# Optimization experiments

Measured on AMD Instinct MI355X. Metric: run time of the kernel, lower is better.

The kernel has to match this reference:

```python
import jax, jax.numpy as jnp
import numpy as np

Q_N, S_N, U_N = 5000, 1000, 2000          # questions, skills, users
NQ = NS = NU = NQ2 = 8                     # neighbor fan-outs
D = 100                                    # emb_dim
AGG_HOPS = 3
RANK_K = 10
S_PER_Q = 4                                # skills per question in qs_table
B, T = 32, 100
NEG = -1e30


def linear(x, W, b):
    return x @ W + b


def _forward(fl, it):
    (uq_table, emb_q, emb_q2, emb_s, emb_u, emb_r,
     w1_q, w2_q, w_c, w_p, w_n,
     lstm_Wih, lstm_Whh, lstm_bih, lstm_bhh,
     fusion_W, fusion_b, agg_W, agg_b, agg_last_W, agg_last_b,
     query_W, query_b, key_W, key_b, attn_W, attn_b) = fl
    (user, question, response, mask,
     q_neighbors, s_neighbors, u_neighbors, q_neighbors_2, skill_idx_table) = it

    K_all = emb_q[question]  # [B,T,D] question embeddings for recap scoring

    def build_nodes(root, tabA, tabB):
        # multi-hop neighbor id gather: [B], [B,n0], [B,n0,n1], [B,n0,n1,n2]
        nodes = [root]
        for i in range(AGG_HOPS):
            tab = tabA if i % 2 == 0 else tabB
            nodes.append(tab[nodes[-1]])
        return nodes

    def aggregate(nodes, embA, embB, weighted):
        embs = [(embA if i % 2 == 0 else embB)[n] for i, n in enumerate(nodes)]
        for i in range(AGG_HOPS):
            for j in range(AGG_HOPS - i):
                nb = embs[j + 1]
                if weighted:  # uq branch: edge weights from dense uq_table
                    self_ids, nb_ids = nodes[j], nodes[j + 1]
                    exp_self = jnp.broadcast_to(self_ids[..., None], nb_ids.shape)
                    uid = exp_self if j % 2 == 0 else nb_ids
                    qid = nb_ids if j % 2 == 0 else exp_self
                    w = uq_table[uid, qid]  # [..., 3]
                    fw = w_c * w[..., 0:1] + w_p * w[..., 1:2] + w_n * w[..., 2:3]
                    nb = nb * fw
                s = nb.mean(axis=-2) + embs[j]
                embs[j] = jax.nn.relu(linear(s, agg_W[j], agg_b[j]))
        return jax.nn.relu(linear(embs[0], agg_last_W, agg_last_b))

    def predict(qs_concat, hist, hist_valid):
        # GIKT-style bi-attention readout (source truncated; see notes)
        k = linear(qs_concat, key_W, key_b)    # [B,Nq,D]
        q = linear(hist, query_W, query_b)     # [B,Nh,D]
        Nq, Nh = k.shape[1], q.shape[1]
        feat = jnp.concatenate([
            jnp.broadcast_to(k[:, :, None, :], (B, Nq, Nh, D)),
            jnp.broadcast_to(q[:, None, :, :], (B, Nq, Nh, D))], axis=-1)
        logits = (feat @ attn_W + attn_b)[..., 0]          # [B,Nq,Nh]
        logits = jnp.where(hist_valid[:, None, :], logits, NEG)
        alpha = jax.nn.softmax(logits.reshape(B, -1), axis=1).reshape(B, Nq, Nh)
        inner = jnp.einsum('bqd,bhd->bqh', qs_concat, hist)
        return jax.nn.sigmoid(jnp.sum(alpha * inner, axis=(1, 2)))

    def step(carry, t):
        h, c, state_hist = carry
        m = mask[:, t][:, None]
        u_t, q_t, r_t = user[:, t], question[:, t], response[:, t]
        emb_qt = jnp.where(m, aggregate(build_nodes(q_t, q_neighbors, s_neighbors), emb_q, emb_s, False), emb_q[q_t])
        emb_qt2 = jnp.where(m, aggregate(build_nodes(u_t, u_neighbors, q_neighbors_2), emb_u, emb_q2, True), emb_q2[q_t])
        emb_hat = w1_q * emb_qt + w2_q * emb_qt2
        e_t = jax.nn.relu(linear(jnp.concatenate([emb_hat, emb_r[r_t]], axis=1), fusion_W, fusion_b))
        # LSTMCell (torch gate order i,f,g,o); dropout is identity in eval
        gates = e_t @ lstm_Wih + lstm_bih + h @ lstm_Whh + lstm_bhh
        ig, fg, gg, og = jnp.split(gates, 4, axis=1)
        c_n = jax.nn.sigmoid(fg) * c + jax.nn.sigmoid(ig) * jnp.tanh(gg)
        h_n = jax.nn.sigmoid(og) * jnp.tanh(c_n)
        h = jnp.where(m, h_n, h)
        c = jnp.where(m, c_n, c)
        state_hist = jax.lax.dynamic_update_slice_in_dim(state_hist, h[:, None, :], t, axis=1)
        # recap: question + related skills, current state + top-k history
        q_next = question[:, t + 1]
        emb_qnext = emb_q[q_next]
        qs_concat = jnp.concatenate([emb_qnext[:, None, :], emb_s[skill_idx_table[q_next]]], axis=1)  # [B,1+S_PER_Q,D]
        scores = jnp.einsum('btd,bd->bt', K_all, emb_qnext)
        scores = jnp.where(jnp.arange(T)[None, :] < t, scores, NEG)  # only past steps
        top_s, idx = jax.lax.top_k(scores, RANK_K)
        sel = jnp.take_along_axis(state_hist, idx[:, :, None], axis=1)  # [B,K,D]
        hist = jnp.concatenate([h[:, None, :], sel], axis=1)             # [B,K+1,D]
        hist_valid = jnp.concatenate([jnp.ones((B, 1), bool), top_s > NEG / 2], axis=1)
        return (h, c, state_hist), predict(qs_concat, hist, hist_valid)

    init = (jnp.zeros((B, D), jnp.float32), jnp.zeros((B, D), jnp.float32),
            jnp.zeros((B, T, D), jnp.float32))
    _, ys = jax.lax.scan(jax.checkpoint(step), init, jnp.arange(T - 1))
    return jnp.zeros((B, T), jnp.float32).at[:, 1:].set(ys.T)


def _p(k, shape, scale=0.1):
    return scale * jax.random.normal(k, shape, dtype=jnp.float32)


def setup_inputs():
    key = jax.random.key(0)
    ks = jax.random.split(key, 24)
    rng = np.random.default_rng(0)
    # qs_table with exactly S_PER_Q distinct skills per question -> static skill index table
    qs_idx = np.argsort(rng.random((Q_N, S_N)), axis=1)[:, :S_PER_Q]
    return dict(
        user=jax.random.randint(ks[0], (B, T), 0, U_N),
        question=jax.random.randint(ks[1], (B, T), 0, Q_N),
        response=jax.random.randint(ks[2], (B, T), 0, 2),
        mask=jnp.ones((B, T), dtype=bool),
        q_neighbors=jax.random.randint(ks[3], (Q_N, NQ), 0, S_N),
        s_neighbors=jax.random.randint(ks[4], (S_N, NS), 0, Q_N),
        u_neighbors=jax.random.randint(ks[5], (U_N, NU), 0, Q_N),
        q_neighbors_2=jax.random.randint(ks[6], (Q_N, NQ2), 0, U_N),
        skill_idx_table=jnp.asarray(qs_idx, dtype=jnp.int32),
        uq_table=jax.random.uniform(ks[7], (U_N, Q_N, 3), dtype=jnp.float32),
        emb_q=_p(ks[8], (Q_N, D)), emb_q2=_p(ks[9], (Q_N, D)),
        emb_s=_p(ks[10], (S_N, D)), emb_u=_p(ks[11], (U_N, D)), emb_r=_p(ks[12], (2, D)),
        w1_q=jnp.asarray(0.5, jnp.float32), w2_q=jnp.asarray(0.5, jnp.float32),
        w_c=jnp.asarray(0.33, jnp.float32), w_p=jnp.asarray(0.33, jnp.float32), w_n=jnp.asarray(0.33, jnp.float32),
        lstm_Wih=_p(ks[13], (D, 4 * D)), lstm_Whh=_p(ks[14], (D, 4 * D)),
        lstm_bih=jnp.zeros(4 * D, jnp.float32), lstm_bhh=jnp.zeros(4 * D, jnp.float32),
        fusion_W=_p(ks[15], (2 * D, D)), fusion_b=jnp.zeros(D, jnp.float32),
        agg_W=_p(ks[16], (AGG_HOPS, D, D)), agg_b=jnp.zeros((AGG_HOPS, D), jnp.float32),
        agg_last_W=_p(ks[17], (D, D)), agg_last_b=jnp.zeros(D, jnp.float32),
        query_W=_p(ks[18], (D, D)), query_b=jnp.zeros(D, jnp.float32),
        key_W=_p(ks[19], (D, D)), key_b=jnp.zeros(D, jnp.float32),
        attn_W=_p(ks[20], (2 * D, 1)), attn_b=jnp.zeros(1, jnp.float32),
    )


def reference(user, question, response, mask, q_neighbors, s_neighbors, u_neighbors,
              q_neighbors_2, skill_idx_table, uq_table, emb_q, emb_q2, emb_s, emb_u, emb_r,
              w1_q, w2_q, w_c, w_p, w_n, lstm_Wih, lstm_Whh, lstm_bih, lstm_bhh,
              fusion_W, fusion_b, agg_W, agg_b, agg_last_W, agg_last_b,
              query_W, query_b, key_W, key_b, attn_W, attn_b):
    fl = (uq_table, emb_q, emb_q2, emb_s, emb_u, emb_r,
          w1_q, w2_q, w_c, w_p, w_n,
          lstm_Wih, lstm_Whh, lstm_bih, lstm_bhh,
          fusion_W, fusion_b, agg_W, agg_b, agg_last_W, agg_last_b,
          query_W, query_b, key_W, key_b, attn_W, attn_b)
    it = (user, question, response, mask,
          q_neighbors, s_neighbors, u_neighbors, q_neighbors_2, skill_idx_table)
    return _forward(fl, it)
```

## Files before the change

### kernel.cpp

```cpp
#include <hip/hip_runtime.h>
#include <math.h>

#define Q_N 5000
#define S_N 1000
#define U_N 2000
#define D   100
#define B   32
#define T   100
#define NBT (B*(T-1))
#define NEG_F (-1e30f)

#define NB_Z2Q ((Q_N+15)/16)
#define NB_Z2U ((U_N+15)/16)
#define NB_Y1Q ((S_N+15)/16)
#define NB_Y1U ((Q_N+15)/16)
#define WB16_U16 (13*400*8)
#define WB16_F   (WB16_U16/2)
#define NB_MK ((NBT+255)/256)
#define NB_PK ((WB16_U16+255)/256)

#define GPROJ_SZ (NBT*4*D)
#define H_SZ     (B*T*D)
#define QAGG_SZ  (Q_N*D)
#define UAGG_SZ  (U_N*D)
#define Z2Q_SZ   (Q_N*D)
#define Z2U_SZ   (U_N*D)
#define Y1Q_SZ   (S_N*D)
#define Y1U_SZ   (Q_N*D)

__device__ __forceinline__ void fma4(float4& a, float s, const float4 w) {
    a.x = fmaf(s, w.x, a.x); a.y = fmaf(s, w.y, a.y);
    a.z = fmaf(s, w.z, a.z); a.w = fmaf(s, w.w, a.w);
}
__device__ __forceinline__ float4 relu4(float4 v) {
    v.x = v.x > 0.f ? v.x : 0.f; v.y = v.y > 0.f ? v.y : 0.f;
    v.z = v.z > 0.f ? v.z : 0.f; v.w = v.w > 0.f ? v.w : 0.f;
    return v;
}
__device__ __forceinline__ float4 add4(float4 a, float4 b) {
    a.x += b.x; a.y += b.y; a.z += b.z; a.w += b.w; return a;
}
__device__ __forceinline__ float b2f_lo(unsigned u) { return __uint_as_float(u << 16); }
__device__ __forceinline__ float b2f_hi(unsigned u) { return __uint_as_float(u & 0xffff0000u); }

template<int K>
__device__ __forceinline__ void mv100_b256(const float* __restrict__ W,
                                           const float* __restrict__ bias,
                                           const float* __restrict__ src,
                                           float* __restrict__ dst,
                                           float* __restrict__ part)
{
    const int tid = threadIdx.x;
    const int c4  = tid & 31;
    const int ks  = tid >> 5;
    const int col0 = (4*c4 < 96) ? 4*c4 : 96;
    float4 acc = {0.f,0.f,0.f,0.f};
#pragma unroll 2
    for (int d = ks*4; d < K; d += 32) {
        const float4 sv = *(const float4*)&src[d];
        const float4 w0 = *(const float4*)&W[(d+0)*D + col0];
        const float4 w1 = *(const float4*)&W[(d+1)*D + col0];
        const float4 w2 = *(const float4*)&W[(d+2)*D + col0];
        const float4 w3 = *(const float4*)&W[(d+3)*D + col0];
        fma4(acc, sv.x, w0); fma4(acc, sv.y, w1);
        fma4(acc, sv.z, w2); fma4(acc, sv.w, w3);
    }
    *(float4*)&part[ks*D + col0] = acc;
    __syncthreads();
    if (tid < D) {
        float v = bias[tid];
#pragma unroll
        for (int k = 0; k < 8; ++k) v += part[k*D + tid];
        dst[tid] = v > 0.f ? v : 0.f;
    }
    __syncthreads();
}

struct __align__(16) Stage16 {
    float x[16*D];
    int   nb[128];
    float fw[128];
};

template<int UQ_MODE>
__device__ __forceinline__ void stage16(Stage16& sh, int row0, int N,
        const float* __restrict__ selfEmb, const float* __restrict__ nbEmb,
        const int* __restrict__ tab,
        const float* __restrict__ uq, float wc, float wp, float wn,
        const float* __restrict__ W, const float* __restrict__ bias,
        float* __restrict__ out)
{
    const int tid = threadIdx.x;
    if (tid < 128) {
        const int i = tid >> 3, k = tid & 7;
        int v = row0 + i; if (v >= N) v = N - 1;
        const int nbv = tab[v*8 + k];
        sh.nb[tid] = nbv;
        float f = 0.125f;
        if (UQ_MODE == 1) {
            const float* w = &uq[(v*Q_N + nbv)*3];
            f = 0.125f*(wc*w[0] + wp*w[1] + wn*w[2]);
        } else if (UQ_MODE == 2) {
            const float* w = &uq[(nbv*Q_N + v)*3];
            f = 0.125f*(wc*w[0] + wp*w[1] + wn*w[2]);
        }
        sh.fw[tid] = f;
    }
    __syncthreads();
    const int c4   = tid & 31;
    const int rowg = tid >> 5;
    const int col0 = (4*c4 < 96) ? 4*c4 : 96;
#pragma unroll
    for (int rr = 0; rr < 2; ++rr) {
        const int i = rowg + 8*rr;
        int v = row0 + i; if (v >= N) v = N - 1;
        float4 acc = *(const float4*)&selfEmb[v*D + col0];
#pragma unroll
        for (int k = 0; k < 8; ++k)
            fma4(acc, sh.fw[i*8 + k], *(const float4*)&nbEmb[sh.nb[i*8 + k]*D + col0]);
        *(float4*)&sh.x[i*D + col0] = acc;
    }
    __syncthreads();
    float4 a0 = {0.f,0.f,0.f,0.f}, a1 = {0.f,0.f,0.f,0.f};
#pragma unroll 1
    for (int d = 0; d < D; d += 4) {
        const float4 w0 = *(const float4*)&W[(d+0)*D + col0];
        const float4 w1 = *(const float4*)&W[(d+1)*D + col0];
        const float4 w2 = *(const float4*)&W[(d+2)*D + col0];
        const float4 w3 = *(const float4*)&W[(d+3)*D + col0];
        const float4 s0 = *(const float4*)&sh.x[rowg*D + d];
        const float4 s1 = *(const float4*)&sh.x[(rowg+8)*D + d];
        fma4(a0, s0.x, w0); fma4(a0, s0.y, w1); fma4(a0, s0.z, w2); fma4(a0, s0.w, w3);
        fma4(a1, s1.x, w0); fma4(a1, s1.y, w1); fma4(a1, s1.z, w2); fma4(a1, s1.w, w3);
    }
    const float4 bb = *(const float4*)&bias[col0];
    {
        int v = row0 + rowg; if (v >= N) v = N - 1;
        *(float4*)&out[v*D + col0] = relu4(add4(a0, bb));
        v = row0 + rowg + 8; if (v >= N) v = N - 1;
        *(float4*)&out[v*D + col0] = relu4(add4(a1, bb));
    }
}

__global__ __launch_bounds__(256, 6)
void kStageA(const int* __restrict__ qnb, const int* __restrict__ snb,
             const int* __restrict__ unb, const int* __restrict__ qnb2,
             const float* __restrict__ emb_q, const float* __restrict__ emb_q2,
             const float* __restrict__ emb_s, const float* __restrict__ emb_u,
             const float* __restrict__ uq,
             const float* __restrict__ wcp, const float* __restrict__ wpp,
             const float* __restrict__ wnp,
             const float* __restrict__ aggW, const float* __restrict__ aggB,
             float* __restrict__ z2q, float* __restrict__ z2u,
             float* __restrict__ y1q0, float* __restrict__ y1u0)
{
    __shared__ Stage16 sh;
    const float wc = wcp[0], wp = wpp[0], wn = wnp[0];
    int b = blockIdx.x;
    if (b < NB_Z2Q) {
        stage16<0>(sh, b*16, Q_N, emb_q, emb_s, qnb, uq, wc, wp, wn,
                   aggW + 2*D*D, aggB + 2*D, z2q);
        return;
    }
    b -= NB_Z2Q;
    if (b < NB_Z2U) {
        stage16<1>(sh, b*16, U_N, emb_u, emb_q2, unb, uq, wc, wp, wn,
                   aggW + 2*D*D, aggB + 2*D, z2u);
        return;
    }
    b -= NB_Z2U;
    if (b < NB_Y1Q) {
        stage16<0>(sh, b*16, S_N, emb_s, emb_q, snb, uq, wc, wp, wn,
                   aggW + 1*D*D, aggB + 1*D, y1q0);
        return;
    }
    b -= NB_Y1Q;
    stage16<2>(sh, b*16, Q_N, emb_q2, emb_u, qnb2, uq, wc, wp, wn,
               aggW + 1*D*D, aggB + 1*D, y1u0);
}

__global__ __launch_bounds__(256, 6)
void kStageB(const int* __restrict__ snb, const int* __restrict__ qnb2,
             const float* __restrict__ uq,
             const float* __restrict__ wcp, const float* __restrict__ wpp,
             const float* __restrict__ wnp,
             const float* __restrict__ aggW, const float* __restrict__ aggB,
             const float* __restrict__ z2q, const float* __restrict__ z2u,
             const float* __restrict__ y1q0, const float* __restrict__ y1u0,
             float* __restrict__ y1q1, float* __restrict__ y1u1)
{
    __shared__ Stage16 sh;
    const float wc = wcp[0], wp = wpp[0], wn = wnp[0];
    int b = blockIdx.x;
    if (b < NB_Y1Q) {
        stage16<0>(sh, b*16, S_N, y1q0, z2q, snb, uq, wc, wp, wn,
                   aggW + 1*D*D, aggB + 1*D, y1q1);
        return;
    }
    b -= NB_Y1Q;
    stage16<2>(sh, b*16, Q_N, y1u0, z2u, qnb2, uq, wc, wp, wn,
               aggW + 1*D*D, aggB + 1*D, y1u1);
}

__global__ void kMarkInit(int* __restrict__ marks)
{
    const int i = blockIdx.x*256 + threadIdx.x;
    if (i < Q_N + U_N) marks[i] = 0;
}

__global__ __launch_bounds__(256)
void kSetup(const int* __restrict__ question, const int* __restrict__ user,
            int* __restrict__ qmark, int* __restrict__ umark,
            const float* __restrict__ Whh, ushort* __restrict__ wb,
            const float* __restrict__ keyW, const float* __restrict__ queryW,
            const float* __restrict__ attnW,
            float* __restrict__ vk, float* __restrict__ vq)
{
    int bkt = blockIdx.x;
    const int tid = threadIdx.x;
    if (bkt < NB_MK) {
        const int bt = bkt*256 + tid;
        if (bt < NBT) {
            const int b = bt / (T-1), t = bt % (T-1);
            qmark[question[b*T + t]] = 1;
            umark[user[b*T + t]] = 1;
        }
        return;
    }
    bkt -= NB_MK;
    if (bkt < NB_PK) {
        const int i = bkt*256 + tid;
        if (i < WB16_U16) {
            const int j  = i & 7;
            const int mc = i >> 3;
            const int m  = mc / 400;
            const int col = mc - m*400;
            const int d  = 8*m + j;
            ushort v = 0;
            if (d < D) {
                unsigned u = __float_as_uint(Whh[d*4*D + col]);
                const unsigned lsb = (u >> 16) & 1u;
                u += 0x7fffu + lsb;
                v = (ushort)(u >> 16);
            }
            wb[i] = v;
        }
        return;
    }
    if (tid < D) {
        float a = 0.f;
        for (int e = 0; e < D; ++e) a = fmaf(keyW[tid*D + e], attnW[e], a);
        vk[tid] = a;
    } else if (tid < 2*D) {
        const int d = tid - D;
        float a = 0.f;
        for (int e = 0; e < D; ++e) a = fmaf(queryW[d*D + e], attnW[D + e], a);
        vq[d] = a;
    }
}

struct __align__(16) RootSh {
    float e0[D];
    float part[8*D];
    int   nb[8];
    float fw[8];
};

template<bool WEIGHTED>
__device__ __forceinline__ void rootchain(RootSh& sh, int root,
        const int* __restrict__ tab,
        const float* __restrict__ selfEmb, const float* __restrict__ lvl1Emb,
        const float* __restrict__ y0, const float* __restrict__ y1,
        const float* __restrict__ W0, const float* __restrict__ b0,
        const float* __restrict__ WL, const float* __restrict__ bL,
        const float* __restrict__ uq, float wc, float wp, float wn,
        float* __restrict__ outrow)
{
    const int tid = threadIdx.x;
    if (tid < 8) {
        const int a = tab[root*8 + tid];
        sh.nb[tid] = a;
        float f = 0.125f;
        if (WEIGHTED) {
            const float* w = &uq[(root*Q_N + a)*3];
            f = 0.125f*(wc*w[0] + wp*w[1] + wn*w[2]);
        }
        sh.fw[tid] = f;
    }
    __syncthreads();
    const int c4 = tid & 31;
    const int col0 = (4*c4 < 96) ? 4*c4 : 96;
    if (tid < 32) {
        float4 acc = *(const float4*)&selfEmb[root*D + col0];
#pragma unroll
        for (int k = 0; k < 8; ++k)
            fma4(acc, sh.fw[k], *(const float4*)&lvl1Emb[sh.nb[k]*D + col0]);
        *(float4*)&sh.e0[col0] = acc;
    }
    __syncthreads();
    mv100_b256<D>(W0, b0, sh.e0, sh.e0, sh.part);
    if (tid < 32) {
        float4 acc = *(const float4*)&sh.e0[col0];
#pragma unroll
        for (int k = 0; k < 8; ++k)
            fma4(acc, sh.fw[k], *(const float4*)&y0[sh.nb[k]*D + col0]);
        *(float4*)&sh.e0[col0] = acc;
    }
    __syncthreads();
    mv100_b256<D>(W0, b0, sh.e0, sh.e0, sh.part);
    if (tid < 32) {
        float4 acc = *(const float4*)&sh.e0[col0];
#pragma unroll
        for (int k = 0; k < 8; ++k)
            fma4(acc, sh.fw[k], *(const float4*)&y1[sh.nb[k]*D + col0]);
        *(float4*)&sh.e0[col0] = acc;
    }
    __syncthreads();
    mv100_b256<D>(W0, b0, sh.e0, sh.e0, sh.part);
    mv100_b256<D>(WL, bL, sh.e0, outrow, sh.part);
}

__global__ __launch_bounds__(256, 6)
void kRoot(const int* __restrict__ qmark, const int* __restrict__ umark,
           const int* __restrict__ qnb, const int* __restrict__ unb,
           const float* __restrict__ emb_q, const float* __restrict__ emb_u,
           const float* __restrict__ emb_s, const float* __restrict__ emb_q2,
           const float* __restrict__ y1q0, const float* __restrict__ y1q1,
           const float* __restrict__ y1u0, const float* __restrict__ y1u1,
           const float* __restrict__ uq,
           const float* __restrict__ wcp, const float* __restrict__ wpp,
           const float* __restrict__ wnp,
           const float* __restrict__ aggW, const float* __restrict__ aggB,
           const float* __restrict__ aggLW, const float* __restrict__ aggLb,
           float* __restrict__ qagg, float* __restrict__ uagg)
{
    __shared__ RootSh sh;
    const int b = blockIdx.x;
    if (b < Q_N) {
        if (!qmark[b]) return;
        rootchain<false>(sh, b, qnb, emb_q, emb_s, y1q0, y1q1,
                         aggW, aggB, aggLW, aggLb,
                         uq, 0.f, 0.f, 0.f, qagg + b*D);
    } else {
        const int u = b - Q_N;
        if (!umark[u]) return;
        rootchain<true>(sh, u, unb, emb_u, emb_q2, y1u0, y1u1,
                        aggW, aggB, aggLW, aggLb,
                        uq, wcp[0], wpp[0], wnp[0], uagg + u*D);
    }
}

__global__ __launch_bounds__(256)
void kFuse(const int* __restrict__ question, const int* __restrict__ user,
           const int* __restrict__ response,
           const float* __restrict__ qagg, const float* __restrict__ uagg,
           const float* __restrict__ emb_r,
           const float* __restrict__ w1p, const float* __restrict__ w2p,
           const float* __restrict__ fusW, const float* __restrict__ fusb,
           const float* __restrict__ Wih, const float* __restrict__ bih,
           float* __restrict__ gproj)
{
    __shared__ __align__(16) float xcat[2*D];
    __shared__ __align__(16) float evec[D];
    __shared__ __align__(16) float part[8*D];
    const int bt = blockIdx.x;
    const int b = bt / (T-1);
    const int t = bt % (T-1);
    const int tid = threadIdx.x;
    const int q = question[b*T + t];
    const int u = user[b*T + t];
    const int r = response[b*T + t];
    const float w1 = w1p[0], w2 = w2p[0];
    const int c4 = tid & 31;
    const int col0 = (4*c4 < 96) ? 4*c4 : 96;
    if (tid < 32) {
        float4 qa = *(const float4*)&qagg[q*D + col0];
        float4 ua = *(const float4*)&uagg[u*D + col0];
        float4 x; x.x = w1*qa.x + w2*ua.x; x.y = w1*qa.y + w2*ua.y;
        x.z = w1*qa.z + w2*ua.z; x.w = w1*qa.w + w2*ua.w;
        *(float4*)&xcat[col0] = x;
    } else if (tid < 64) {
        *(float4*)&xcat[D + col0] = *(const float4*)&emb_r[r*D + col0];
    }
    __syncthreads();
    mv100_b256<2*D>(fusW, fusb, xcat, evec, part);

    const int ks = tid >> 7, cw = tid & 127;
    if (cw < D) {
        float4 acc = {0.f,0.f,0.f,0.f};
#pragma unroll 5
        for (int dd = 0; dd < D/2; ++dd) {
            const int d = ks*(D/2) + dd;
            fma4(acc, evec[d], *(const float4*)&Wih[d*4*D + 4*cw]);
        }
        *(float4*)&part[ks*4*D + 4*cw] = acc;
    }
    __syncthreads();
    for (int i = tid; i < 4*D; i += 256) {
        gproj[bt*4*D + i] = part[i] + part[4*D + i] + bih[i];
    }
}

#define KB_LDW(m) const uint4 W##m = wp[m*400 + col];
#define KB_FMA(m) { const float4 h0 = *(const float4*)&hbuf[8*m]; \
                    const float4 h1 = *(const float4*)&hbuf[8*m + 4]; \
    a0 = fmaf(h0.x, b2f_lo(W##m.x), a0); \
    a1 = fmaf(h0.y, b2f_hi(W##m.x), a1); \
    a2 = fmaf(h0.z, b2f_lo(W##m.y), a2); \
    a3 = fmaf(h0.w, b2f_hi(W##m.y), a3); \
    a0 = fmaf(h1.x, b2f_lo(W##m.z), a0); \
    a1 = fmaf(h1.y, b2f_hi(W##m.z), a1); \
    a2 = fmaf(h1.z, b2f_lo(W##m.w), a2); \
    a3 = fmaf(h1.w, b2f_hi(W##m.w), a3); }

__global__ __attribute__((amdgpu_flat_work_group_size(512, 512)))
           __attribute__((amdgpu_waves_per_eu(2, 2)))
void kB(const float* __restrict__ gproj, const ushort* __restrict__ wb,
        const float* __restrict__ bhh, float* __restrict__ H)
{
    __shared__ __align__(16) float hbuf[104];
    __shared__ float gates[4*D];
    const int b = blockIdx.x;
    const int tid = threadIdx.x;
    const bool on = tid < 4*D;
    const int col = on ? tid : (4*D - 1);
    const float bb = bhh[col];
    const bool isG = (col >= 2*D) && (col < 3*D);
    const uint4* wp = (const uint4*)wb;
    KB_LDW(0)  KB_LDW(1)  KB_LDW(2)  KB_LDW(3)  KB_LDW(4)  KB_LDW(5)
    KB_LDW(6)  KB_LDW(7)  KB_LDW(8)  KB_LDW(9)  KB_LDW(10) KB_LDW(11)
    KB_LDW(12)
    float creg = 0.f;
    if (tid < 104) hbuf[tid] = 0.f;
    float g = on ? gproj[(b*(T-1) + 0)*4*D + col] : 0.f;
    __syncthreads();
#pragma unroll 1
    for (int t = 0; t < T-1; ++t) {
        if (on) {
            float a0 = g + bb, a1 = 0.f, a2 = 0.f, a3 = 0.f;
            KB_FMA(0)  KB_FMA(1)  KB_FMA(2)  KB_FMA(3)  KB_FMA(4)  KB_FMA(5)
            KB_FMA(6)  KB_FMA(7)  KB_FMA(8)  KB_FMA(9)  KB_FMA(10) KB_FMA(11)
            KB_FMA(12)
            const float tot = (a0 + a1) + (a2 + a3);
            gates[col] = isG ? tanhf(tot) : 1.f/(1.f + expf(-tot));
        }
        __syncthreads();
        if (t + 1 < T-1 && on) g = gproj[(b*(T-1) + t + 1)*4*D + col];
        if (tid < D) {
            const float ig = gates[tid];
            const float fg = gates[D   + tid];
            const float gg = gates[2*D + tid];
            const float og = gates[3*D + tid];
            const float cn = fg*creg + ig*gg;
            const float hn = og*tanhf(cn);
            creg = cn;
            hbuf[tid] = hn;
            H[(b*T + t)*D + tid] = hn;
        }
        __syncthreads();
    }
}

__global__ __launch_bounds__(128)
void kC(const int* __restrict__ question, const int* __restrict__ skill_tab,
        const float* __restrict__ emb_q, const float* __restrict__ emb_s,
        const float* __restrict__ H, const float* __restrict__ vk,
        const float* __restrict__ vq, float* __restrict__ out)
{
    __shared__ __align__(16) float qs[5*D];
    __shared__ __align__(16) float hist[11*D];
    __shared__ float scores[T];
    __shared__ float kdot[5], qdot[11];
    __shared__ int   topi[10];
    __shared__ float topv[10];
    const int blk = blockIdx.x;
    const int b = blk / (T-1);
    const int t = blk % (T-1);
    const int tid = threadIdx.x;
    const int qn = question[b*T + t + 1];

    for (int i = tid; i < 5*D; i += 128) {
        const int rr = i / D, d = i % D;
        if (rr == 0) qs[i] = emb_q[qn*D + d];
        else         qs[i] = emb_s[skill_tab[qn*4 + (rr-1)]*D + d];
    }
    __syncthreads();

    for (int tau = tid; tau < T; tau += 128) {
        float sc = NEG_F;
        if (tau < t) {
            const float4* rowp = (const float4*)&emb_q[question[b*T + tau]*D];
            float acc = 0.f;
#pragma unroll 1
            for (int d4 = 0; d4 < D/4; ++d4) {
                const float4 a  = rowp[d4];
                const float4 qv = *(const float4*)&qs[d4*4];
                acc += a.x*qv.x + a.y*qv.y + a.z*qv.z + a.w*qv.w;
            }
            sc = acc;
        }
        scores[tau] = sc;
    }
    __syncthreads();

    for (int k = 0; k < 10; ++k) {
        if (tid < 64) {
            float v = scores[tid]; int idx = tid;
            if (tid + 64 < T) {
                const float v2 = scores[tid + 64];
                if (v2 > v) { v = v2; idx = tid + 64; }
            }
            for (int off = 32; off > 0; off >>= 1) {
                const float ov = __shfl_xor(v, off);
                const int   oi = __shfl_xor(idx, off);
                if (ov > v || (ov == v && oi < idx)) { v = ov; idx = oi; }
            }
            if (tid == 0) { topi[k] = idx; topv[k] = v; scores[idx] = NEG_F; }
        }
        __syncthreads();
    }

    for (int i = tid; i < 11*D; i += 128) {
        const int j = i / D, d = i % D;
        float v;
        if (j == 0) v = H[(b*T + t)*D + d];
        else        v = (topv[j-1] > -5e29f) ? H[(b*T + topi[j-1])*D + d] : 0.f;
        hist[i] = v;
    }
    __syncthreads();

    {
        const int dj = tid >> 3, ks = tid & 7;
        const float* vec = (dj < 5) ? &qs[dj*D] : &hist[(dj-5)*D];
        const float* vv  = (dj < 5) ? vk : vq;
        float a = 0.f;
#pragma unroll
        for (int d = ks; d < D; d += 8) a = fmaf(vec[d], vv[d], a);
        a += __shfl_xor(a, 1); a += __shfl_xor(a, 2); a += __shfl_xor(a, 4);
        if (ks == 0) { if (dj < 5) kdot[dj] = a; else qdot[dj-5] = a; }
    }
    __syncthreads();

    if (tid < 64) {
        const int i = tid / 11, j = tid - i*11;
        const bool act = tid < 55;
        const bool valid = act && (j == 0 || topv[j-1] > -5e29f);
        float logit = valid ? (kdot[i] + qdot[j]) : NEG_F;
        float mx = logit;
        for (int off = 32; off > 0; off >>= 1) mx = fmaxf(mx, __shfl_xor(mx, off));
        const float e = valid ? expf(logit - mx) : 0.f;
        float inner = 0.f;
        if (act) {
#pragma unroll
            for (int d4 = 0; d4 < D/4; ++d4) {
                const float4 a4 = *(const float4*)&qs[i*D + d4*4];
                const float4 h4 = *(const float4*)&hist[j*D + d4*4];
                inner += a4.x*h4.x + a4.y*h4.y + a4.z*h4.z + a4.w*h4.w;
            }
        }
        float num = e * inner;
        float den = e;
        for (int off = 32; off > 0; off >>= 1) {
            num += __shfl_xor(num, off);
            den += __shfl_xor(den, off);
        }
        if (tid == 0) {
            out[b*T + t + 1] = 1.f/(1.f + expf(-(num/den)));
            if (t == 0) out[b*T] = 0.f;
        }
    }
}

extern "C" void kernel_launch(void* const* d_in, const int* in_sizes, int n_in,
                              void* d_out, int out_size, void* d_ws, size_t ws_size,
                              hipStream_t stream)
{
    const int*   user     = (const int*)d_in[0];
    const int*   question = (const int*)d_in[1];
    const int*   response = (const int*)d_in[2];
    const int*   qnb   = (const int*)d_in[4];
    const int*   snb   = (const int*)d_in[5];
    const int*   unb   = (const int*)d_in[6];
    const int*   qnb2  = (const int*)d_in[7];
    const int*   skill = (const int*)d_in[8];
    const float* uq    = (const float*)d_in[9];
    const float* emb_q  = (const float*)d_in[10];
    const float* emb_q2 = (const float*)d_in[11];
    const float* emb_s  = (const float*)d_in[12];
    const float* emb_u  = (const float*)d_in[13];
    const float* emb_r  = (const float*)d_in[14];
    const float* w1 = (const float*)d_in[15];
    const float* w2 = (const float*)d_in[16];
    const float* wc = (const float*)d_in[17];
    const float* wp = (const float*)d_in[18];
    const float* wn = (const float*)d_in[19];
    const float* Wih = (const float*)d_in[20];
    const float* Whh = (const float*)d_in[21];
    const float* bih = (const float*)d_in[22];
    const float* bhh = (const float*)d_in[23];
    const float* fusW = (const float*)d_in[24];
    const float* fusb = (const float*)d_in[25];
    const float* aggW = (const float*)d_in[26];
    const float* aggB = (const float*)d_in[27];
    const float* aggLW = (const float*)d_in[28];
    const float* aggLb = (const float*)d_in[29];
    const float* queryW = (const float*)d_in[30];
    const float* keyW   = (const float*)d_in[32];
    const float* attnW  = (const float*)d_in[34];

    float* ws    = (float*)d_ws;
    float* gproj = ws;
    float* H     = gproj + GPROJ_SZ;
    float* vk    = H + H_SZ;
    float* vq    = vk + D;
    float* qagg  = vq + D;
    float* uagg  = qagg + QAGG_SZ;
    float* z2q   = uagg + UAGG_SZ;
    float* z2u   = z2q + Z2Q_SZ;
    float* y1q0  = z2u + Z2U_SZ;
    float* y1q1  = y1q0 + Y1Q_SZ;
    float* y1u0  = y1q1 + Y1Q_SZ;
    float* y1u1  = y1u0 + Y1U_SZ;
    ushort* wb16 = (ushort*)(y1u1 + Y1U_SZ);
    int*   qmark = (int*)((float*)wb16 + WB16_F);
    int*   umark = qmark + Q_N;
    float* out   = (float*)d_out;

    const size_t need = (size_t)(GPROJ_SZ + H_SZ + 2*D + QAGG_SZ + UAGG_SZ
                       + Z2Q_SZ + Z2U_SZ + 2*Y1Q_SZ + 2*Y1U_SZ + WB16_F)*sizeof(float)
                       + (size_t)(Q_N + U_N)*sizeof(int);
    if (ws_size < need) return;

    kMarkInit<<<dim3((Q_N + U_N + 255)/256), dim3(256), 0, stream>>>(qmark);
    kSetup<<<dim3(NB_MK + NB_PK + 1), dim3(256), 0, stream>>>(
        question, user, qmark, umark, Whh, wb16, keyW, queryW, attnW, vk, vq);
    kStageA<<<dim3(NB_Z2Q + NB_Z2U + NB_Y1Q + NB_Y1U), dim3(256), 0, stream>>>(
        qnb, snb, unb, qnb2, emb_q, emb_q2, emb_s, emb_u, uq, wc, wp, wn,
        aggW, aggB, z2q, z2u, y1q0, y1u0);
    kStageB<<<dim3(NB_Y1Q + NB_Y1U), dim3(256), 0, stream>>>(
        snb, qnb2, uq, wc, wp, wn, aggW, aggB, z2q, z2u, y1q0, y1u0, y1q1, y1u1);
    kRoot<<<dim3(Q_N + U_N), dim3(256), 0, stream>>>(
        qmark, umark, qnb, unb, emb_q, emb_u, emb_s, emb_q2,
        y1q0, y1q1, y1u0, y1u1, uq, wc, wp, wn,
        aggW, aggB, aggLW, aggLb, qagg, uagg);
    kFuse<<<dim3(NBT), dim3(256), 0, stream>>>(question, user, response, qagg, uagg,
        emb_r, w1, w2, fusW, fusb, Wih, bih, gproj);
    kB<<<dim3(B), dim3(512), 0, stream>>>(gproj, wb16, bhh, H);
    kC<<<dim3(NBT), dim3(128), 0, stream>>>(question, skill, emb_q, emb_s, H, vk, vq, out);
}
```

Measured before the change: 238.4 us.

## Batch 16 rows per fusion block and stage aggregation weights in LDS

kFuse now handles 16 (b,t) rows per block rather than one. Each block does register-blocked matmuls, so every fusion and input-projection weight load is reused across 16 rows instead of being reread once per row. kRoot copies the 100x100 aggregation weight into shared memory once per block and reuses it for three matvecs. The larger LDS footprint lowers the occupancy hint from 6 to 3 blocks. The price is lower occupancy in kRoot and fewer blocks in kFuse; NB_FU assumes NBT divides by 16 (3168/16 = 198 does).

```diff
diff --git a/kernel.cpp b/kernel.cpp
--- a/kernel.cpp
+++ b/kernel.cpp
@@ -18,6 +18,7 @@
 #define WB16_F   (WB16_U16/2)
 #define NB_MK ((NBT+255)/256)
 #define NB_PK ((WB16_U16+255)/256)
+#define NB_FU (NBT/16)
 
 #define GPROJ_SZ (NBT*4*D)
 #define H_SZ     (B*T*D)
@@ -260,6 +261,7 @@
 }
 
 struct __align__(16) RootSh {
+    float w0[D*D];
     float e0[D];
     float part[8*D];
     int   nb[8];
@@ -277,6 +279,12 @@
         float* __restrict__ outrow)
 {
     const int tid = threadIdx.x;
+    {
+        const float4* src = (const float4*)W0;
+        float4* dst = (float4*)sh.w0;
+#pragma unroll 1
+        for (int i = tid; i < D*D/4; i += 256) dst[i] = src[i];
+    }
     if (tid < 8) {
         const int a = tab[root*8 + tid];
         sh.nb[tid] = a;
@@ -298,7 +306,7 @@
         *(float4*)&sh.e0[col0] = acc;
     }
     __syncthreads();
-    mv100_b256<D>(W0, b0, sh.e0, sh.e0, sh.part);
+    mv100_b256<D>(sh.w0, b0, sh.e0, sh.e0, sh.part);
     if (tid < 32) {
         float4 acc = *(const float4*)&sh.e0[col0];
 #pragma unroll
@@ -307,7 +315,7 @@
         *(float4*)&sh.e0[col0] = acc;
     }
     __syncthreads();
-    mv100_b256<D>(W0, b0, sh.e0, sh.e0, sh.part);
+    mv100_b256<D>(sh.w0, b0, sh.e0, sh.e0, sh.part);
     if (tid < 32) {
         float4 acc = *(const float4*)&sh.e0[col0];
 #pragma unroll
@@ -316,11 +324,11 @@
         *(float4*)&sh.e0[col0] = acc;
     }
     __syncthreads();
-    mv100_b256<D>(W0, b0, sh.e0, sh.e0, sh.part);
+    mv100_b256<D>(sh.w0, b0, sh.e0, sh.e0, sh.part);
     mv100_b256<D>(WL, bL, sh.e0, outrow, sh.part);
 }
 
-__global__ __launch_bounds__(256, 6)
+__global__ __launch_bounds__(256, 3)
 void kRoot(const int* __restrict__ qmark, const int* __restrict__ umark,
            const int* __restrict__ qnb, const int* __restrict__ unb,
            const float* __restrict__ emb_q, const float* __restrict__ emb_u,
@@ -360,44 +368,83 @@
            const float* __restrict__ Wih, const float* __restrict__ bih,
            float* __restrict__ gproj)
 {
-    __shared__ __align__(16) float xcat[2*D];
-    __shared__ __align__(16) float evec[D];
-    __shared__ __align__(16) float part[8*D];
-    const int bt = blockIdx.x;
-    const int b = bt / (T-1);
-    const int t = bt % (T-1);
+    __shared__ __align__(16) float x[16][2*D];
+    __shared__ __align__(16) float evecT[D][20];
+    const int row0 = blockIdx.x * 16;
     const int tid = threadIdx.x;
-    const int q = question[b*T + t];
-    const int u = user[b*T + t];
-    const int r = response[b*T + t];
     const float w1 = w1p[0], w2 = w2p[0];
-    const int c4 = tid & 31;
-    const int col0 = (4*c4 < 96) ? 4*c4 : 96;
-    if (tid < 32) {
-        float4 qa = *(const float4*)&qagg[q*D + col0];
-        float4 ua = *(const float4*)&uagg[u*D + col0];
-        float4 x; x.x = w1*qa.x + w2*ua.x; x.y = w1*qa.y + w2*ua.y;
-        x.z = w1*qa.z + w2*ua.z; x.w = w1*qa.w + w2*ua.w;
-        *(float4*)&xcat[col0] = x;
-    } else if (tid < 64) {
-        *(float4*)&xcat[D + col0] = *(const float4*)&emb_r[r*D + col0];
-    }
-    __syncthreads();
-    mv100_b256<2*D>(fusW, fusb, xcat, evec, part);
-
-    const int ks = tid >> 7, cw = tid & 127;
-    if (cw < D) {
-        float4 acc = {0.f,0.f,0.f,0.f};
-#pragma unroll 5
-        for (int dd = 0; dd < D/2; ++dd) {
-            const int d = ks*(D/2) + dd;
-            fma4(acc, evec[d], *(const float4*)&Wih[d*4*D + 4*cw]);
-        }
-        *(float4*)&part[ks*4*D + 4*cw] = acc;
-    }
-    __syncthreads();
-    for (int i = tid; i < 4*D; i += 256) {
-        gproj[bt*4*D + i] = part[i] + part[4*D + i] + bih[i];
+#pragma unroll 1
+    for (int idx = tid; idx < 16*50; idx += 256) {
+        const int i = idx / 50, c4 = idx - i*50;
+        const int bt = row0 + i;
+        const int b = bt / (T-1), t = bt - b*(T-1);
+        const int col0 = c4*4;
+        float4 v;
+        if (col0 < D) {
+            const int q = question[b*T + t];
+            const int u = user[b*T + t];
+            const float4 qa = *(const float4*)&qagg[q*D + col0];
+            const float4 ua = *(const float4*)&uagg[u*D + col0];
+            v.x = w1*qa.x + w2*ua.x; v.y = w1*qa.y + w2*ua.y;
+            v.z = w1*qa.z + w2*ua.z; v.w = w1*qa.w + w2*ua.w;
+        } else {
+            const int r = response[b*T + t];
+            v = *(const float4*)&emb_r[r*D + (col0 - D)];
+        }
+        *(float4*)&x[i][col0] = v;
+    }
+    __syncthreads();
+    {
+        const int c4 = tid & 31;
+        const int rowg = tid >> 5;
+        const int col0 = (4*c4 < 96) ? 4*c4 : 96;
+        float4 a0 = {0.f,0.f,0.f,0.f}, a1 = {0.f,0.f,0.f,0.f};
+#pragma unroll 2
+        for (int d = 0; d < 2*D; d += 4) {
+            const float4 w0v = *(const float4*)&fusW[(d+0)*D + col0];
+            const float4 w1v = *(const float4*)&fusW[(d+1)*D + col0];
+            const float4 w2v = *(const float4*)&fusW[(d+2)*D + col0];
+            const float4 w3v = *(const float4*)&fusW[(d+3)*D + col0];
+            const float4 s0 = *(const float4*)&x[rowg][d];
+            const float4 s1 = *(const float4*)&x[rowg+8][d];
+            fma4(a0, s0.x, w0v); fma4(a0, s0.y, w1v);
+            fma4(a0, s0.z, w2v); fma4(a0, s0.w, w3v);
+            fma4(a1, s1.x, w0v); fma4(a1, s1.y, w1v);
+            fma4(a1, s1.z, w2v); fma4(a1, s1.w, w3v);
+        }
+        const float4 bb = *(const float4*)&fusb[col0];
+        a0 = relu4(add4(a0, bb)); a1 = relu4(add4(a1, bb));
+        evecT[col0+0][rowg] = a0.x; evecT[col0+1][rowg] = a0.y;
+        evecT[col0+2][rowg] = a0.z; evecT[col0+3][rowg] = a0.w;
+        evecT[col0+0][rowg+8] = a1.x; evecT[col0+1][rowg+8] = a1.y;
+        evecT[col0+2][rowg+8] = a1.z; evecT[col0+3][rowg+8] = a1.w;
+    }
+    __syncthreads();
+    {
+        const int c  = tid & 127;
+        const int rh = tid >> 7;
+        if (c < D) {
+            const int col0 = 4*c;
+            float4 acc[8];
+#pragma unroll
+            for (int r = 0; r < 8; ++r) acc[r] = {0.f,0.f,0.f,0.f};
+#pragma unroll 2
+            for (int k = 0; k < D; ++k) {
+                const float4 wv = *(const float4*)&Wih[k*4*D + col0];
+                const float4 e0 = *(const float4*)&evecT[k][rh*8];
+                const float4 e1 = *(const float4*)&evecT[k][rh*8 + 4];
+                fma4(acc[0], e0.x, wv); fma4(acc[1], e0.y, wv);
+                fma4(acc[2], e0.z, wv); fma4(acc[3], e0.w, wv);
+                fma4(acc[4], e1.x, wv); fma4(acc[5], e1.y, wv);
+                fma4(acc[6], e1.z, wv); fma4(acc[7], e1.w, wv);
+            }
+            const float4 bb = *(const float4*)&bih[col0];
+#pragma unroll
+            for (int r = 0; r < 8; ++r) {
+                const int bt = row0 + rh*8 + r;
+                *(float4*)&gproj[bt*4*D + col0] = add4(acc[r], bb);
+            }
+        }
     }
 }
 
@@ -643,7 +690,7 @@
         qmark, umark, qnb, unb, emb_q, emb_u, emb_s, emb_q2,
         y1q0, y1q1, y1u0, y1u1, uq, wc, wp, wn,
         aggW, aggB, aggLW, aggLb, qagg, uagg);
-    kFuse<<<dim3(NBT), dim3(256), 0, stream>>>(question, user, response, qagg, uagg,
+    kFuse<<<dim3(NB_FU), dim3(256), 0, stream>>>(question, user, response, qagg, uagg,
         emb_r, w1, w2, fusW, fusb, Wih, bih, gproj);
     kB<<<dim3(B), dim3(512), 0, stream>>>(gproj, wb16, bhh, H);
     kC<<<dim3(NBT), dim3(128), 0, stream>>>(question, skill, emb_q, emb_s, H, vk, vq, out);
```

After: 249.4 us. 4.6% more time.
